# Performance work log

Hardware: AMD Instinct MI355X
Metric: run time of the kernel (lower is better)

The kernel has to match this reference:

```python
import jax, jax.numpy as jnp
import numpy as np

N, E, B = 50000, 600000, 64
C_IN, H, C_OUT, L = 128, 128, 64, 3
BN_EPS = 1e-5


def setup_inputs() -> dict:
    key = jax.random.key(0)
    ks = iter(jax.random.split(key, 40))

    def w(shape, fan_in):
        return jax.random.normal(next(ks), shape, jnp.float32) / np.sqrt(fan_in).astype(np.float32)

    return {
        "x": jax.random.normal(next(ks), (N, C_IN), jnp.float32),
        "edge_index": jax.random.randint(next(ks), (2, E), 0, N),
        "batch": jnp.sort(jax.random.randint(next(ks), (N,), 0, B)),
        # GINConv MLPs: Linear(in,h) -> BN -> ReLU -> Linear(h,h)   (stacked over L; C_IN == H)
        "convW1": w((L, C_IN, H), C_IN), "convb1": jnp.zeros((L, H), jnp.float32),
        "bn_g": jnp.ones((L, H), jnp.float32), "bn_b": jnp.zeros((L, H), jnp.float32),
        "convW2": w((L, H, H), H), "convb2": jnp.zeros((L, H), jnp.float32),
        # reconstruction head: Linear(h,h)-ReLU-Linear(h,h)-ReLU-Linear(h,4)-ReLU
        "recW1": w((H, H), H), "recb1": jnp.zeros((H,), jnp.float32),
        "recW2": w((H, H), H), "recb2": jnp.zeros((H,), jnp.float32),
        "recW3": w((H, 4), H), "recb3": jnp.zeros((4,), jnp.float32),
        # final MLP([h,h,out], norm=None): Linear(h,h)-ReLU-(dropout, eval=identity)-Linear(h,out)
        "mlpW1": w((H, H), H), "mlpb1": jnp.zeros((H,), jnp.float32),
        "mlpW2": w((H, C_OUT), H), "mlpb2": jnp.zeros((C_OUT,), jnp.float32),
    }


def reference(x, edge_index, batch, convW1, convb1, bn_g, bn_b, convW2, convb2,
              recW1, recb1, recW2, recb2, recW3, recb3, mlpW1, mlpb1, mlpW2, mlpb2):
    src, dst = edge_index[0], edge_index[1]
    for l in range(L):
        # GIN aggregation: out_i = nn((1+eps)*x_i + sum_{j->i} x_j), eps = 0
        agg = jax.ops.segment_sum(x[src], dst, num_segments=N)  # [N, d]
        h = (x + agg) @ convW1[l] + convb1[l]                   # [N, H]
        mu = h.mean(axis=0)
        var = jnp.var(h, axis=0)                                # biased, torch BN train mode
        h = bn_g[l] * (h - mu) * jax.lax.rsqrt(var + BN_EPS) + bn_b[l]
        h = jax.nn.relu(h) @ convW2[l] + convb2[l]
        x = jax.nn.relu(h)                                      # outer .relu() in forward
    # reconstruction branch on node features
    x_rec = jax.nn.relu(x @ recW1 + recb1)
    x_rec = jax.nn.relu(x_rec @ recW2 + recb2)
    x_rec = jax.nn.relu(x_rec @ recW3 + recb3)                  # [N, 4]
    # global_add_pool keyed by graph id
    pooled = jax.ops.segment_sum(x, batch, num_segments=B)      # [B, H]
    out = jax.nn.relu(pooled @ mlpW1 + mlpb1) @ mlpW2 + mlpb2   # [B, C_OUT]
    return (out, x_rec)
```

## Files before the change

### kernel.cpp

```cpp
#include <hip/hip_runtime.h>

#define NN 50000
#define EE 600000
#define BB 64
#define CH 128
#define LL 3
#define NGB 391
#define NSB 196
#define NPB 392

typedef unsigned short u16;
typedef unsigned int u32;
typedef short s16x8 __attribute__((ext_vector_type(8)));
typedef float f32x4 __attribute__((ext_vector_type(4)));

__device__ __forceinline__ u16 f2b(float f) {
    u32 x = __float_as_uint(f);
    return (u16)((x + 0x7FFFu + ((x >> 16) & 1u)) >> 16);
}
__device__ __forceinline__ float b2f(u16 u) {
    return __uint_as_float(((u32)u) << 16);
}

__global__ __launch_bounds__(256) void k_zero2(int* __restrict__ deg,
                                               float* __restrict__ pooled) {
    int i = blockIdx.x * 256 + threadIdx.x;
    if (i < NN) deg[i] = 0;
    int j = i - NN;
    if (j >= 0 && j < BB * CH) pooled[j] = 0.f;
}

__global__ __launch_bounds__(256) void k_count(const int* __restrict__ ei,
                                               int* __restrict__ deg) {
    int e = blockIdx.x * 256 + threadIdx.x;
    if (e < EE) atomicAdd(&deg[ei[EE + e]], 1);
}

__global__ __launch_bounds__(256) void k_scanA(const int* __restrict__ deg,
                                               int* __restrict__ bsum) {
    __shared__ int sm[256];
    int i = blockIdx.x * 256 + threadIdx.x;
    sm[threadIdx.x] = (i < NN) ? deg[i] : 0;
    __syncthreads();
    for (int off = 128; off > 0; off >>= 1) {
        if (threadIdx.x < off) sm[threadIdx.x] += sm[threadIdx.x + off];
        __syncthreads();
    }
    if (threadIdx.x == 0) bsum[blockIdx.x] = sm[0];
}

__global__ __launch_bounds__(256) void k_scanB(const int* __restrict__ deg,
                                               const int* __restrict__ bsum,
                                               int* __restrict__ rowptr,
                                               int* __restrict__ cur) {
    __shared__ int sb[256], sd[256];
    int t = threadIdx.x;
    sb[t] = (t < NSB) ? bsum[t] : 0;
    __syncthreads();
    for (int off = 1; off < 256; off <<= 1) {
        int v = (t >= off) ? sb[t - off] : 0;
        __syncthreads();
        sb[t] += v;
        __syncthreads();
    }
    int blockOff = (blockIdx.x == 0) ? 0 : sb[blockIdx.x - 1];
    int i = blockIdx.x * 256 + t;
    int d = (i < NN) ? deg[i] : 0;
    sd[t] = d;
    __syncthreads();
    for (int off = 1; off < 256; off <<= 1) {
        int v = (t >= off) ? sd[t - off] : 0;
        __syncthreads();
        sd[t] += v;
        __syncthreads();
    }
    int excl = blockOff + sd[t] - d;
    if (i < NN) { rowptr[i] = excl; cur[i] = excl; }
    if (i == NN - 1) rowptr[NN] = excl + d;
}

__global__ __launch_bounds__(256) void k_fill(const int* __restrict__ ei,
                                              int* __restrict__ cur,
                                              int* __restrict__ perm) {
    int e = blockIdx.x * 256 + threadIdx.x;
    if (e < EE) {
        int dst = ei[EE + e];
        int idx = atomicAdd(&cur[dst], 1);
        perm[idx] = ei[e];
    }
}

__global__ __launch_bounds__(256) void k_cvt(const float* __restrict__ x,
                                             u16* __restrict__ y) {
    long base = (long)(blockIdx.x * 256 + threadIdx.x) * 8;
    if (base < (long)NN * CH) {
        float4 f0 = *(const float4*)(x + base);
        float4 f1 = *(const float4*)(x + base + 4);
        union { u16 pk[8]; uint4 v; } uu;
        uu.pk[0] = f2b(f0.x); uu.pk[1] = f2b(f0.y);
        uu.pk[2] = f2b(f0.z); uu.pk[3] = f2b(f0.w);
        uu.pk[4] = f2b(f1.x); uu.pk[5] = f2b(f1.y);
        uu.pk[6] = f2b(f1.z); uu.pk[7] = f2b(f1.w);
        *(uint4*)(y + base) = uu.v;
    }
}

__global__ __launch_bounds__(256) void k_gather(const u16* __restrict__ x,
                                                const int* __restrict__ rowptr,
                                                const int* __restrict__ perm,
                                                u16* __restrict__ y) {
    int dst = blockIdx.x * 16 + (threadIdx.x >> 4);
    if (dst >= NN) return;
    int lane = threadIdx.x & 15;
    int co = lane * 8;
    int beg = rowptr[dst], end = rowptr[dst + 1];
    union { u16 pk[8]; uint4 v; } uu;
    uu.v = *(const uint4*)(x + (long)dst * CH + co);
    float a[8], b[8];
#pragma unroll
    for (int j = 0; j < 8; ++j) { a[j] = b2f(uu.pk[j]); b[j] = 0.f; }
    int e = beg;
    for (; e + 1 < end; e += 2) {
        int s0 = perm[e], s1 = perm[e + 1];
        union { u16 pk[8]; uint4 v; } v0, v1;
        v0.v = *(const uint4*)(x + (long)s0 * CH + co);
        v1.v = *(const uint4*)(x + (long)s1 * CH + co);
#pragma unroll
        for (int j = 0; j < 8; ++j) { a[j] += b2f(v0.pk[j]); b[j] += b2f(v1.pk[j]); }
    }
    if (e < end) {
        int s0 = perm[e];
        union { u16 pk[8]; uint4 v; } v0;
        v0.v = *(const uint4*)(x + (long)s0 * CH + co);
#pragma unroll
        for (int j = 0; j < 8; ++j) a[j] += b2f(v0.pk[j]);
    }
    union { u16 pk[8]; uint4 v; } ov;
#pragma unroll
    for (int j = 0; j < 8; ++j) ov.pk[j] = f2b(a[j] + b[j]);
    *(uint4*)(y + (long)dst * CH + co) = ov.v;
}

__global__ __launch_bounds__(256) void k_transpose_all(
    const float* __restrict__ cW1, const float* __restrict__ cW2,
    const float* __restrict__ rW1, const float* __restrict__ rW2,
    const float* __restrict__ rW3, u16* __restrict__ Wt) {
    int idx = blockIdx.x * 256 + threadIdx.x;
    if (idx < 8 * 16384) {
        int slot = idx >> 14;
        int wi = idx & 16383;
        int k = wi >> 7, n = wi & 127;
        const float* src = slot < 3 ? cW1 + slot * 16384
                         : slot < 6 ? cW2 + (slot - 3) * 16384
                         : slot == 6 ? rW1 : rW2;
        Wt[slot * 16384 + n * 128 + k] = f2b(src[wi]);
    } else if (idx < 9 * 16384) {
        int j = idx - 8 * 16384;
        int n = j >> 7, k = j & 127;
        Wt[8 * 16384 + j] = (n < 4) ? f2b(rW3[k * 4 + n]) : (u16)0;
    }
}

__device__ __forceinline__ void stageB8(const u16* __restrict__ Wt, u16* sB,
                                        int s, int rr) {
#pragma unroll
    for (int it = 0; it < 8; ++it) {
        int n = it * 16 + rr;
        uint4 u = *(const uint4*)(Wt + n * CH + 8 * s);
        *(uint4*)(&sB[n * CH + ((s ^ (n & 15)) * 8)]) = u;
    }
}

__device__ __forceinline__ void mfma8(const u16* sA, const u16* sB,
                                      f32x4 acc[2][8], int wv, int quad, int l16) {
    f32x4 z = {0.f, 0.f, 0.f, 0.f};
#pragma unroll
    for (int m = 0; m < 2; ++m)
#pragma unroll
        for (int t = 0; t < 8; ++t) acc[m][t] = z;
    const u16* pa0 = sA + (wv * 32 + l16) * CH;
    const u16* pa1 = pa0 + 16 * CH;
#pragma unroll
    for (int kc = 0; kc < 4; ++kc) {
        int off = (((kc << 2) | quad) ^ l16) << 3;
        s16x8 a0 = *(const s16x8*)(pa0 + off);
        s16x8 a1 = *(const s16x8*)(pa1 + off);
#pragma unroll
        for (int t = 0; t < 8; ++t) {
            s16x8 bfr = *(const s16x8*)(sB + (t * 16 + l16) * CH + off);
            acc[0][t] = __builtin_amdgcn_mfma_f32_16x16x32_bf16(a0, bfr, acc[0][t], 0, 0, 0);
            acc[1][t] = __builtin_amdgcn_mfma_f32_16x16x32_bf16(a1, bfr, acc[1][t], 0, 0, 0);
        }
    }
}

__device__ __forceinline__ void biasrelu(f32x4 acc[2][8],
                                         const float* __restrict__ bias, int l16) {
#pragma unroll
    for (int t = 0; t < 8; ++t) {
        float bv = bias[t * 16 + l16];
#pragma unroll
        for (int m = 0; m < 2; ++m)
#pragma unroll
            for (int r = 0; r < 4; ++r)
                acc[m][t][r] = fmaxf(acc[m][t][r] + bv, 0.f);
    }
}

__device__ __forceinline__ void restage(const f32x4 acc[2][8], u16* sA,
                                        int wv, int quad, int l16) {
#pragma unroll
    for (int t = 0; t < 8; ++t) {
        int chunk = (t << 1) | (l16 >> 3);
        int o7 = l16 & 7;
#pragma unroll
        for (int m = 0; m < 2; ++m)
#pragma unroll
            for (int r = 0; r < 4; ++r) {
                int lr = wv * 32 + m * 16 + quad * 4 + r;
                sA[lr * CH + ((chunk ^ (lr & 15)) << 3) + o7] = f2b(acc[m][t][r]);
            }
    }
}

template <bool ABF16, bool BN, bool RELU, bool STATS, bool OUTBF16>
__global__ __launch_bounds__(256) void k_gemm(
    const void* __restrict__ Ap, const u16* __restrict__ Wt,
    const float* __restrict__ bias, const float* __restrict__ scale,
    const float* __restrict__ shift, void* __restrict__ Cp,
    float* __restrict__ pstats, int M) {
    __shared__ u16 sA[128 * CH];
    __shared__ u16 sB[128 * CH];
    const int tid = threadIdx.x;
    const int s = tid & 15;
    const int rr = tid >> 4;
    const int r0 = blockIdx.x * 128;

    float sc[8], sh[8];
    if constexpr (BN) {
#pragma unroll
        for (int j = 0; j < 8; ++j) {
            sc[j] = scale[8 * s + j];
            sh[j] = shift[8 * s + j];
        }
    }

    stageB8(Wt, sB, s, rr);
#pragma unroll
    for (int it = 0; it < 8; ++it) {
        int lr = it * 16 + rr;
        int gr = r0 + lr;
        union { u16 pk[8]; uint4 v; } uu;
        if (gr < M) {
            if constexpr (ABF16) {
                uu.v = *(const uint4*)((const u16*)Ap + (long)gr * CH + 8 * s);
                if constexpr (BN) {
#pragma unroll
                    for (int j = 0; j < 8; ++j)
                        uu.pk[j] = f2b(fmaxf(b2f(uu.pk[j]) * sc[j] + sh[j], 0.f));
                }
            } else {
                const float* Af = (const float*)Ap + (long)gr * CH + 8 * s;
                float4 f0 = *(const float4*)Af;
                float4 f1 = *(const float4*)(Af + 4);
                float vj[8] = {f0.x, f0.y, f0.z, f0.w, f1.x, f1.y, f1.z, f1.w};
#pragma unroll
                for (int j = 0; j < 8; ++j) {
                    float v = vj[j];
                    if constexpr (BN) v = fmaxf(v * sc[j] + sh[j], 0.f);
                    uu.pk[j] = f2b(v);
                }
            }
        } else {
#pragma unroll
            for (int j = 0; j < 8; ++j) uu.pk[j] = 0;
        }
        *(uint4*)(&sA[lr * CH + ((s ^ (lr & 15)) * 8)]) = uu.v;
    }
    __syncthreads();

    const int lane = tid & 63;
    const int wv = tid >> 6;
    const int quad = lane >> 4;
    const int l16 = lane & 15;

    f32x4 acc[2][8];
    mfma8(sA, sB, acc, wv, quad, l16);

    float ss[8], qq[8];
    if constexpr (STATS) {
#pragma unroll
        for (int t = 0; t < 8; ++t) { ss[t] = 0.f; qq[t] = 0.f; }
    }

#pragma unroll
    for (int t = 0; t < 8; ++t) {
        int col = t * 16 + l16;
        float bv = bias[col];
#pragma unroll
        for (int m = 0; m < 2; ++m) {
            int rbase = r0 + wv * 32 + m * 16 + quad * 4;
#pragma unroll
            for (int r = 0; r < 4; ++r) {
                int row = rbase + r;
                if (row < M) {
                    float v = acc[m][t][r] + bv;
                    if constexpr (STATS) { ss[t] += v; qq[t] += v * v; }
                    if constexpr (RELU) v = fmaxf(v, 0.f);
                    if constexpr (OUTBF16)
                        ((u16*)Cp)[(long)row * CH + col] = f2b(v);
                    else
                        ((float*)Cp)[(long)row * CH + col] = v;
                }
            }
        }
    }

    if constexpr (STATS) {
#pragma unroll
        for (int t = 0; t < 8; ++t) {
            ss[t] += __shfl_xor(ss[t], 16);
            ss[t] += __shfl_xor(ss[t], 32);
            qq[t] += __shfl_xor(qq[t], 16);
            qq[t] += __shfl_xor(qq[t], 32);
        }
        float* red = (float*)sA;
        __syncthreads();
        if (lane < 16) {
#pragma unroll
            for (int t = 0; t < 8; ++t) {
                red[wv * 256 + t * 16 + l16] = ss[t];
                red[wv * 256 + 128 + t * 16 + l16] = qq[t];
            }
        }
        __syncthreads();
        float v = red[tid] + red[256 + tid] + red[512 + tid] + red[768 + tid];
        pstats[(long)blockIdx.x * 256 + tid] = v;
    }
}

__global__ __launch_bounds__(256) void k_tail(
    const u16* __restrict__ h16, const u16* __restrict__ Wt,
    const float* __restrict__ cb2, const float* __restrict__ scale,
    const float* __restrict__ shift, const float* __restrict__ rb1,
    const float* __restrict__ rb2, const float* __restrict__ rb3,
    u16* __restrict__ xc, float* __restrict__ x_rec) {
    __shared__ u16 sA[128 * CH];
    __shared__ u16 sB[128 * CH];
    const int tid = threadIdx.x;
    const int s = tid & 15, rr = tid >> 4;
    const int r0 = blockIdx.x * 128;
    const int lane = tid & 63, wv = tid >> 6, quad = lane >> 4, l16 = lane & 15;

    float sc[8], sh[8];
#pragma unroll
    for (int j = 0; j < 8; ++j) { sc[j] = scale[8 * s + j]; sh[j] = shift[8 * s + j]; }
    stageB8(Wt + 5 * 16384, sB, s, rr);
#pragma unroll
    for (int it = 0; it < 8; ++it) {
        int lr = it * 16 + rr, gr = r0 + lr;
        union { u16 pk[8]; uint4 v; } uu;
        if (gr < NN) {
            uu.v = *(const uint4*)(h16 + (long)gr * CH + 8 * s);
#pragma unroll
            for (int j = 0; j < 8; ++j)
                uu.pk[j] = f2b(fmaxf(b2f(uu.pk[j]) * sc[j] + sh[j], 0.f));
        } else {
#pragma unroll
            for (int j = 0; j < 8; ++j) uu.pk[j] = 0;
        }
        *(uint4*)(&sA[lr * CH + ((s ^ (lr & 15)) * 8)]) = uu.v;
    }
    __syncthreads();
    f32x4 acc[2][8];
    mfma8(sA, sB, acc, wv, quad, l16);
    biasrelu(acc, cb2, l16);
#pragma unroll
    for (int t = 0; t < 8; ++t) {
        int col = t * 16 + l16;
#pragma unroll
        for (int m = 0; m < 2; ++m)
#pragma unroll
            for (int r = 0; r < 4; ++r) {
                int row = r0 + wv * 32 + m * 16 + quad * 4 + r;
                if (row < NN) xc[(long)row * CH + col] = f2b(acc[m][t][r]);
            }
    }
    __syncthreads();
    restage(acc, sA, wv, quad, l16);
    stageB8(Wt + 6 * 16384, sB, s, rr);
    __syncthreads();
    mfma8(sA, sB, acc, wv, quad, l16);
    biasrelu(acc, rb1, l16);
    __syncthreads();
    restage(acc, sA, wv, quad, l16);
    stageB8(Wt + 7 * 16384, sB, s, rr);
    __syncthreads();
    mfma8(sA, sB, acc, wv, quad, l16);
    biasrelu(acc, rb2, l16);
    __syncthreads();
    restage(acc, sA, wv, quad, l16);
    {
        int n = rr;
        uint4 u = *(const uint4*)(Wt + 8 * 16384 + n * CH + 8 * s);
        *(uint4*)(&sB[n * CH + ((s ^ (n & 15)) * 8)]) = u;
    }
    __syncthreads();
    f32x4 a4[2];
    a4[0] = (f32x4){0.f, 0.f, 0.f, 0.f};
    a4[1] = (f32x4){0.f, 0.f, 0.f, 0.f};
    {
        const u16* pa0 = sA + (wv * 32 + l16) * CH;
        const u16* pa1 = pa0 + 16 * CH;
#pragma unroll
        for (int kc = 0; kc < 4; ++kc) {
            int off = (((kc << 2) | quad) ^ l16) << 3;
            s16x8 a0 = *(const s16x8*)(pa0 + off);
            s16x8 a1 = *(const s16x8*)(pa1 + off);
            s16x8 bfr = *(const s16x8*)(sB + l16 * CH + off);
            a4[0] = __builtin_amdgcn_mfma_f32_16x16x32_bf16(a0, bfr, a4[0], 0, 0, 0);
            a4[1] = __builtin_amdgcn_mfma_f32_16x16x32_bf16(a1, bfr, a4[1], 0, 0, 0);
        }
    }
    if (l16 < 4) {
        float bv = rb3[l16];
#pragma unroll
        for (int m = 0; m < 2; ++m)
#pragma unroll
            for (int r = 0; r < 4; ++r) {
                int row = r0 + wv * 32 + m * 16 + quad * 4 + r;
                if (row < NN) x_rec[(long)row * 4 + l16] = fmaxf(a4[m][r] + bv, 0.f);
            }
    }
}

__global__ __launch_bounds__(256) void k_bnparam(const float* __restrict__ pstats,
                                                 const float* __restrict__ g,
                                                 const float* __restrict__ b,
                                                 float* __restrict__ scale,
                                                 float* __restrict__ shift) {
    __shared__ float sm[256];
    int t = threadIdx.x;
    float acc = 0.f;
    for (int blk = 0; blk < NGB; ++blk) acc += pstats[blk * 256 + t];
    sm[t] = acc;
    __syncthreads();
    if (t < 128) {
        float mu = sm[t] / (float)NN;
        float var = sm[128 + t] / (float)NN - mu * mu;
        float rstd = rsqrtf(var + 1e-5f);
        float gg = g[t], bb = b[t];
        scale[t] = gg * rstd;
        shift[t] = bb - mu * gg * rstd;
    }
}

__global__ __launch_bounds__(256) void k_pool(const u16* __restrict__ x,
                                              const int* __restrict__ batch,
                                              float* __restrict__ pooled) {
    int r0 = blockIdx.x * 128;
    if (r0 >= NN) return;
    int rend = r0 + 128 < NN ? r0 + 128 : NN;
    int c = threadIdx.x & 127;
    int half = threadIdx.x >> 7;
    int r = r0 + half;
    if (r >= rend) return;
    int g = batch[r];
    float s = 0.f;
    for (; r < rend; r += 2) {
        int gg = batch[r];
        if (gg != g) {
            unsafeAtomicAdd(pooled + g * CH + c, s);
            s = 0.f;
            g = gg;
        }
        s += b2f(x[(long)r * CH + c]);
    }
    unsafeAtomicAdd(pooled + g * CH + c, s);
}

__global__ __launch_bounds__(128) void k_mlp(const float* __restrict__ pooled,
                                             const float* __restrict__ W1,
                                             const float* __restrict__ b1,
                                             const float* __restrict__ W2,
                                             const float* __restrict__ b2,
                                             float* __restrict__ out) {
    __shared__ float p[128], t1[128];
    int b = blockIdx.x, t = threadIdx.x;
    p[t] = pooled[b * CH + t];
    __syncthreads();
    float acc = b1[t];
    for (int k = 0; k < 128; ++k) acc += p[k] * W1[k * 128 + t];
    t1[t] = fmaxf(acc, 0.f);
    __syncthreads();
    if (t < 64) {
        float o = b2[t];
        for (int k = 0; k < 128; ++k) o += t1[k] * W2[k * 64 + t];
        out[b * 64 + t] = o;
    }
}

extern "C" void kernel_launch(void* const* d_in, const int* in_sizes, int n_in,
                              void* d_out, int out_size, void* d_ws, size_t ws_size,
                              hipStream_t stream) {
    const float* x_in   = (const float*)d_in[0];
    const int*   ei     = (const int*)d_in[1];
    const int*   batch  = (const int*)d_in[2];
    const float* convW1 = (const float*)d_in[3];
    const float* convb1 = (const float*)d_in[4];
    const float* bn_g   = (const float*)d_in[5];
    const float* bn_b   = (const float*)d_in[6];
    const float* convW2 = (const float*)d_in[7];
    const float* convb2 = (const float*)d_in[8];
    const float* recW1  = (const float*)d_in[9];
    const float* recb1  = (const float*)d_in[10];
    const float* recW2  = (const float*)d_in[11];
    const float* recb2  = (const float*)d_in[12];
    const float* recW3  = (const float*)d_in[13];
    const float* recb3  = (const float*)d_in[14];
    const float* mlpW1  = (const float*)d_in[15];
    const float* mlpb1  = (const float*)d_in[16];
    const float* mlpW2  = (const float*)d_in[17];
    const float* mlpb2  = (const float*)d_in[18];

    float* out   = (float*)d_out;
    float* x_rec = out + 4096;

    char* w = (char*)d_ws;
    u16*   x16    = (u16*)w;    w += (size_t)NN * CH * 2;
    u16*   y16    = (u16*)w;    w += (size_t)NN * CH * 2;
    u16*   h16    = (u16*)w;    w += (size_t)NN * CH * 2;
    u16*   xc     = (u16*)w;    w += (size_t)NN * CH * 2;
    u16*   Wt     = (u16*)w;    w += (size_t)9 * 16384 * 2;
    float* pstats = (float*)w;  w += (size_t)NGB * 256 * 4;
    float* scale  = (float*)w;  w += 128 * 4;
    float* shift  = (float*)w;  w += 128 * 4;
    float* pooled = (float*)w;  w += (size_t)BB * CH * 4;
    int*   deg    = (int*)w;    w += (size_t)NN * 4;
    int*   bsum   = (int*)w;    w += (size_t)NSB * 4;
    int*   rowptr = (int*)w;    w += (size_t)(NN + 1) * 4;
    int*   cur    = (int*)w;    w += (size_t)NN * 4;
    int*   perm   = (int*)w;    w += (size_t)EE * 4;

    dim3 b256(256), b128(128);

    k_zero2<<<228, b256, 0, stream>>>(deg, pooled);
    k_count<<<2344, b256, 0, stream>>>(ei, deg);
    k_scanA<<<NSB, b256, 0, stream>>>(deg, bsum);
    k_scanB<<<NSB, b256, 0, stream>>>(deg, bsum, rowptr, cur);
    k_fill<<<2344, b256, 0, stream>>>(ei, cur, perm);
    k_cvt<<<3125, b256, 0, stream>>>(x_in, x16);
    k_transpose_all<<<576, b256, 0, stream>>>(convW1, convW2, recW1, recW2, recW3, Wt);

    const u16* cur_x = x16;
    for (int l = 0; l < LL; ++l) {
        k_gather<<<3125, b256, 0, stream>>>(cur_x, rowptr, perm, y16);
        k_gemm<true, false, false, true, true><<<NGB, b256, 0, stream>>>(
            y16, Wt + l * 16384, convb1 + l * 128, nullptr, nullptr, h16, pstats, NN);
        k_bnparam<<<1, b256, 0, stream>>>(pstats, bn_g + l * 128, bn_b + l * 128, scale, shift);
        if (l < LL - 1) {
            k_gemm<true, true, true, false, true><<<NGB, b256, 0, stream>>>(
                h16, Wt + (3 + l) * 16384, convb2 + l * 128, scale, shift, xc, nullptr, NN);
            cur_x = xc;
        }
    }
    k_tail<<<NGB, b256, 0, stream>>>(h16, Wt, convb2 + 2 * 128, scale, shift,
                                     recb1, recb2, recb3, xc, x_rec);
    k_pool<<<NPB, b256, 0, stream>>>(xc, batch, pooled);
    k_mlp<<<64, b128, 0, stream>>>(pooled, mlpW1, mlpb1, mlpW2, mlpb2, out);
}
```

Baseline: 431.6 us.

## Fuse per-layer GEMMs and BN stats via grid barrier in a single kernel

Replaces the per-layer sequence (GEMM1 with partial stats, single-block BN param reduction, GEMM2 with BN+ReLU) with one persistent kernel per layer. Each block keeps its GEMM1 accumulators in registers, atomically adds column sums into a global stats buffer, waits at a software grid barrier, then applies BN+ReLU and runs GEMM2 (plus the reconstruction head on the last layer). This removes the h16 intermediate round-trip through memory and two kernel launches per layer. The barrier depends on all 391 blocks being co-resident, which launch bounds of 2 blocks per CU are meant to ensure, and any block that is not resident would deadlock.

```diff
diff --git a/kernel.cpp b/kernel.cpp
--- a/kernel.cpp
+++ b/kernel.cpp
@@ -23,11 +23,17 @@
 }
 
 __global__ __launch_bounds__(256) void k_zero2(int* __restrict__ deg,
-                                               float* __restrict__ pooled) {
+                                               float* __restrict__ pooled,
+                                               float* __restrict__ gstats,
+                                               int* __restrict__ bar) {
     int i = blockIdx.x * 256 + threadIdx.x;
     if (i < NN) deg[i] = 0;
     int j = i - NN;
     if (j >= 0 && j < BB * CH) pooled[j] = 0.f;
+    int k = j - BB * CH;
+    if (k >= 0 && k < 3 * 256) gstats[k] = 0.f;
+    int l = k - 3 * 256;
+    if (l >= 0 && l < 4) bar[l] = 0;
 }
 
 __global__ __launch_bounds__(256) void k_count(const int* __restrict__ ei,
@@ -223,128 +229,25 @@
     }
 }
 
-template <bool ABF16, bool BN, bool RELU, bool STATS, bool OUTBF16>
-__global__ __launch_bounds__(256) void k_gemm(
-    const void* __restrict__ Ap, const u16* __restrict__ Wt,
-    const float* __restrict__ bias, const float* __restrict__ scale,
-    const float* __restrict__ shift, void* __restrict__ Cp,
-    float* __restrict__ pstats, int M) {
-    __shared__ u16 sA[128 * CH];
-    __shared__ u16 sB[128 * CH];
-    const int tid = threadIdx.x;
-    const int s = tid & 15;
-    const int rr = tid >> 4;
-    const int r0 = blockIdx.x * 128;
-
-    float sc[8], sh[8];
-    if constexpr (BN) {
-#pragma unroll
-        for (int j = 0; j < 8; ++j) {
-            sc[j] = scale[8 * s + j];
-            sh[j] = shift[8 * s + j];
-        }
-    }
-
-    stageB8(Wt, sB, s, rr);
-#pragma unroll
-    for (int it = 0; it < 8; ++it) {
-        int lr = it * 16 + rr;
-        int gr = r0 + lr;
-        union { u16 pk[8]; uint4 v; } uu;
-        if (gr < M) {
-            if constexpr (ABF16) {
-                uu.v = *(const uint4*)((const u16*)Ap + (long)gr * CH + 8 * s);
-                if constexpr (BN) {
-#pragma unroll
-                    for (int j = 0; j < 8; ++j)
-                        uu.pk[j] = f2b(fmaxf(b2f(uu.pk[j]) * sc[j] + sh[j], 0.f));
-                }
-            } else {
-                const float* Af = (const float*)Ap + (long)gr * CH + 8 * s;
-                float4 f0 = *(const float4*)Af;
-                float4 f1 = *(const float4*)(Af + 4);
-                float vj[8] = {f0.x, f0.y, f0.z, f0.w, f1.x, f1.y, f1.z, f1.w};
-#pragma unroll
-                for (int j = 0; j < 8; ++j) {
-                    float v = vj[j];
-                    if constexpr (BN) v = fmaxf(v * sc[j] + sh[j], 0.f);
-                    uu.pk[j] = f2b(v);
-                }
-            }
-        } else {
-#pragma unroll
-            for (int j = 0; j < 8; ++j) uu.pk[j] = 0;
-        }
-        *(uint4*)(&sA[lr * CH + ((s ^ (lr & 15)) * 8)]) = uu.v;
-    }
-    __syncthreads();
-
-    const int lane = tid & 63;
-    const int wv = tid >> 6;
-    const int quad = lane >> 4;
-    const int l16 = lane & 15;
-
-    f32x4 acc[2][8];
-    mfma8(sA, sB, acc, wv, quad, l16);
-
-    float ss[8], qq[8];
-    if constexpr (STATS) {
-#pragma unroll
-        for (int t = 0; t < 8; ++t) { ss[t] = 0.f; qq[t] = 0.f; }
-    }
-
-#pragma unroll
-    for (int t = 0; t < 8; ++t) {
-        int col = t * 16 + l16;
-        float bv = bias[col];
-#pragma unroll
-        for (int m = 0; m < 2; ++m) {
-            int rbase = r0 + wv * 32 + m * 16 + quad * 4;
-#pragma unroll
-            for (int r = 0; r < 4; ++r) {
-                int row = rbase + r;
-                if (row < M) {
-                    float v = acc[m][t][r] + bv;
-                    if constexpr (STATS) { ss[t] += v; qq[t] += v * v; }
-                    if constexpr (RELU) v = fmaxf(v, 0.f);
-                    if constexpr (OUTBF16)
-                        ((u16*)Cp)[(long)row * CH + col] = f2b(v);
-                    else
-                        ((float*)Cp)[(long)row * CH + col] = v;
-                }
-            }
-        }
-    }
-
-    if constexpr (STATS) {
-#pragma unroll
-        for (int t = 0; t < 8; ++t) {
-            ss[t] += __shfl_xor(ss[t], 16);
-            ss[t] += __shfl_xor(ss[t], 32);
-            qq[t] += __shfl_xor(qq[t], 16);
-            qq[t] += __shfl_xor(qq[t], 32);
-        }
-        float* red = (float*)sA;
-        __syncthreads();
-        if (lane < 16) {
-#pragma unroll
-            for (int t = 0; t < 8; ++t) {
-                red[wv * 256 + t * 16 + l16] = ss[t];
-                red[wv * 256 + 128 + t * 16 + l16] = qq[t];
-            }
-        }
-        __syncthreads();
-        float v = red[tid] + red[256 + tid] + red[512 + tid] + red[768 + tid];
-        pstats[(long)blockIdx.x * 256 + tid] = v;
-    }
-}
-
-__global__ __launch_bounds__(256) void k_tail(
-    const u16* __restrict__ h16, const u16* __restrict__ Wt,
-    const float* __restrict__ cb2, const float* __restrict__ scale,
-    const float* __restrict__ shift, const float* __restrict__ rb1,
-    const float* __restrict__ rb2, const float* __restrict__ rb3,
-    u16* __restrict__ xc, float* __restrict__ x_rec) {
+__device__ __forceinline__ void grid_barrier(int* bar, int tid) {
+    __syncthreads();
+    if (tid == 0) {
+        __hip_atomic_fetch_add(bar, 1, __ATOMIC_ACQ_REL, __HIP_MEMORY_SCOPE_AGENT);
+        while (__hip_atomic_load(bar, __ATOMIC_ACQUIRE, __HIP_MEMORY_SCOPE_AGENT) < NGB) {
+            __builtin_amdgcn_s_sleep(8);
+        }
+    }
+    __syncthreads();
+}
+
+template <bool LAST>
+__global__ __launch_bounds__(256, 2) void k_layer(
+    const u16* __restrict__ y16, const u16* __restrict__ Wt, int layer,
+    const float* __restrict__ cb1, const float* __restrict__ cb2,
+    const float* __restrict__ g, const float* __restrict__ bbeta,
+    float* __restrict__ gstats, int* __restrict__ bar, u16* __restrict__ xc,
+    const float* __restrict__ rb1, const float* __restrict__ rb2,
+    const float* __restrict__ rb3, float* __restrict__ x_rec) {
     __shared__ u16 sA[128 * CH];
     __shared__ u16 sB[128 * CH];
     const int tid = threadIdx.x;
@@ -352,19 +255,13 @@
     const int r0 = blockIdx.x * 128;
     const int lane = tid & 63, wv = tid >> 6, quad = lane >> 4, l16 = lane & 15;
 
-    float sc[8], sh[8];
-#pragma unroll
-    for (int j = 0; j < 8; ++j) { sc[j] = scale[8 * s + j]; sh[j] = shift[8 * s + j]; }
-    stageB8(Wt + 5 * 16384, sB, s, rr);
+    stageB8(Wt + layer * 16384, sB, s, rr);
 #pragma unroll
     for (int it = 0; it < 8; ++it) {
         int lr = it * 16 + rr, gr = r0 + lr;
         union { u16 pk[8]; uint4 v; } uu;
         if (gr < NN) {
-            uu.v = *(const uint4*)(h16 + (long)gr * CH + 8 * s);
-#pragma unroll
-            for (int j = 0; j < 8; ++j)
-                uu.pk[j] = f2b(fmaxf(b2f(uu.pk[j]) * sc[j] + sh[j], 0.f));
+            uu.v = *(const uint4*)(y16 + (long)gr * CH + 8 * s);
         } else {
 #pragma unroll
             for (int j = 0; j < 8; ++j) uu.pk[j] = 0;
@@ -373,6 +270,69 @@
     }
     __syncthreads();
     f32x4 acc[2][8];
+    mfma8(sA, sB, acc, wv, quad, l16);
+
+    float ss[8], qq[8];
+#pragma unroll
+    for (int t = 0; t < 8; ++t) {
+        float bv = cb1[t * 16 + l16];
+        ss[t] = 0.f; qq[t] = 0.f;
+#pragma unroll
+        for (int m = 0; m < 2; ++m) {
+            int rbase = r0 + wv * 32 + m * 16 + quad * 4;
+#pragma unroll
+            for (int r = 0; r < 4; ++r) {
+                float v = acc[m][t][r] + bv;
+                acc[m][t][r] = v;
+                if (rbase + r < NN) { ss[t] += v; qq[t] += v * v; }
+            }
+        }
+    }
+#pragma unroll
+    for (int t = 0; t < 8; ++t) {
+        ss[t] += __shfl_xor(ss[t], 16);
+        ss[t] += __shfl_xor(ss[t], 32);
+        qq[t] += __shfl_xor(qq[t], 16);
+        qq[t] += __shfl_xor(qq[t], 32);
+    }
+    float* red = (float*)sA;
+    __syncthreads();
+    if (lane < 16) {
+#pragma unroll
+        for (int t = 0; t < 8; ++t) {
+            red[wv * 256 + t * 16 + l16] = ss[t];
+            red[wv * 256 + 128 + t * 16 + l16] = qq[t];
+        }
+    }
+    __syncthreads();
+    unsafeAtomicAdd(&gstats[tid],
+                    red[tid] + red[256 + tid] + red[512 + tid] + red[768 + tid]);
+
+    grid_barrier(bar, tid);
+
+#pragma unroll
+    for (int t = 0; t < 8; ++t) {
+        int col = t * 16 + l16;
+        float sum = __hip_atomic_load(&gstats[col], __ATOMIC_RELAXED,
+                                      __HIP_MEMORY_SCOPE_AGENT);
+        float sq = __hip_atomic_load(&gstats[128 + col], __ATOMIC_RELAXED,
+                                     __HIP_MEMORY_SCOPE_AGENT);
+        float mu = sum / (float)NN;
+        float var = sq / (float)NN - mu * mu;
+        float rstd = rsqrtf(var + 1e-5f);
+        float sc = g[col] * rstd;
+        float sh = bbeta[col] - mu * sc;
+#pragma unroll
+        for (int m = 0; m < 2; ++m)
+#pragma unroll
+            for (int r = 0; r < 4; ++r)
+                acc[m][t][r] = fmaxf(acc[m][t][r] * sc + sh, 0.f);
+    }
+
+    __syncthreads();
+    restage(acc, sA, wv, quad, l16);
+    stageB8(Wt + (3 + layer) * 16384, sB, s, rr);
+    __syncthreads();
     mfma8(sA, sB, acc, wv, quad, l16);
     biasrelu(acc, cb2, l16);
 #pragma unroll
@@ -386,30 +346,31 @@
                 if (row < NN) xc[(long)row * CH + col] = f2b(acc[m][t][r]);
             }
     }
-    __syncthreads();
-    restage(acc, sA, wv, quad, l16);
-    stageB8(Wt + 6 * 16384, sB, s, rr);
-    __syncthreads();
-    mfma8(sA, sB, acc, wv, quad, l16);
-    biasrelu(acc, rb1, l16);
-    __syncthreads();
-    restage(acc, sA, wv, quad, l16);
-    stageB8(Wt + 7 * 16384, sB, s, rr);
-    __syncthreads();
-    mfma8(sA, sB, acc, wv, quad, l16);
-    biasrelu(acc, rb2, l16);
-    __syncthreads();
-    restage(acc, sA, wv, quad, l16);
-    {
-        int n = rr;
-        uint4 u = *(const uint4*)(Wt + 8 * 16384 + n * CH + 8 * s);
-        *(uint4*)(&sB[n * CH + ((s ^ (n & 15)) * 8)]) = u;
-    }
-    __syncthreads();
-    f32x4 a4[2];
-    a4[0] = (f32x4){0.f, 0.f, 0.f, 0.f};
-    a4[1] = (f32x4){0.f, 0.f, 0.f, 0.f};
-    {
+
+    if constexpr (LAST) {
+        __syncthreads();
+        restage(acc, sA, wv, quad, l16);
+        stageB8(Wt + 6 * 16384, sB, s, rr);
+        __syncthreads();
+        mfma8(sA, sB, acc, wv, quad, l16);
+        biasrelu(acc, rb1, l16);
+        __syncthreads();
+        restage(acc, sA, wv, quad, l16);
+        stageB8(Wt + 7 * 16384, sB, s, rr);
+        __syncthreads();
+        mfma8(sA, sB, acc, wv, quad, l16);
+        biasrelu(acc, rb2, l16);
+        __syncthreads();
+        restage(acc, sA, wv, quad, l16);
+        {
+            int n = rr;
+            uint4 u = *(const uint4*)(Wt + 8 * 16384 + n * CH + 8 * s);
+            *(uint4*)(&sB[n * CH + ((s ^ (n & 15)) * 8)]) = u;
+        }
+        __syncthreads();
+        f32x4 a4[2];
+        a4[0] = (f32x4){0.f, 0.f, 0.f, 0.f};
+        a4[1] = (f32x4){0.f, 0.f, 0.f, 0.f};
         const u16* pa0 = sA + (wv * 32 + l16) * CH;
         const u16* pa1 = pa0 + 16 * CH;
 #pragma unroll
@@ -421,37 +382,16 @@
             a4[0] = __builtin_amdgcn_mfma_f32_16x16x32_bf16(a0, bfr, a4[0], 0, 0, 0);
             a4[1] = __builtin_amdgcn_mfma_f32_16x16x32_bf16(a1, bfr, a4[1], 0, 0, 0);
         }
-    }
-    if (l16 < 4) {
-        float bv = rb3[l16];
-#pragma unroll
-        for (int m = 0; m < 2; ++m)
-#pragma unroll
-            for (int r = 0; r < 4; ++r) {
-                int row = r0 + wv * 32 + m * 16 + quad * 4 + r;
-                if (row < NN) x_rec[(long)row * 4 + l16] = fmaxf(a4[m][r] + bv, 0.f);
-            }
-    }
-}
-
-__global__ __launch_bounds__(256) void k_bnparam(const float* __restrict__ pstats,
-                                                 const float* __restrict__ g,
-                                                 const float* __restrict__ b,
-                                                 float* __restrict__ scale,
-                                                 float* __restrict__ shift) {
-    __shared__ float sm[256];
-    int t = threadIdx.x;
-    float acc = 0.f;
-    for (int blk = 0; blk < NGB; ++blk) acc += pstats[blk * 256 + t];
-    sm[t] = acc;
-    __syncthreads();
-    if (t < 128) {
-        float mu = sm[t] / (float)NN;
-        float var = sm[128 + t] / (float)NN - mu * mu;
-        float rstd = rsqrtf(var + 1e-5f);
-        float gg = g[t], bb = b[t];
-        scale[t] = gg * rstd;
-        shift[t] = bb - mu * gg * rstd;
+        if (l16 < 4) {
+            float bv = rb3[l16];
+#pragma unroll
+            for (int m = 0; m < 2; ++m)
+#pragma unroll
+                for (int r = 0; r < 4; ++r) {
+                    int row = r0 + wv * 32 + m * 16 + quad * 4 + r;
+                    if (row < NN) x_rec[(long)row * 4 + l16] = fmaxf(a4[m][r] + bv, 0.f);
+                }
+        }
     }
 }
 
@@ -529,12 +469,10 @@
     char* w = (char*)d_ws;
     u16*   x16    = (u16*)w;    w += (size_t)NN * CH * 2;
     u16*   y16    = (u16*)w;    w += (size_t)NN * CH * 2;
-    u16*   h16    = (u16*)w;    w += (size_t)NN * CH * 2;
     u16*   xc     = (u16*)w;    w += (size_t)NN * CH * 2;
     u16*   Wt     = (u16*)w;    w += (size_t)9 * 16384 * 2;
-    float* pstats = (float*)w;  w += (size_t)NGB * 256 * 4;
-    float* scale  = (float*)w;  w += 128 * 4;
-    float* shift  = (float*)w;  w += 128 * 4;
+    float* gstats = (float*)w;  w += (size_t)3 * 256 * 4;
+    int*   bar    = (int*)w;    w += 4 * 4;
     float* pooled = (float*)w;  w += (size_t)BB * CH * 4;
     int*   deg    = (int*)w;    w += (size_t)NN * 4;
     int*   bsum   = (int*)w;    w += (size_t)NSB * 4;
@@ -544,7 +482,7 @@
 
     dim3 b256(256), b128(128);
 
-    k_zero2<<<228, b256, 0, stream>>>(deg, pooled);
+    k_zero2<<<231, b256, 0, stream>>>(deg, pooled, gstats, bar);
     k_count<<<2344, b256, 0, stream>>>(ei, deg);
     k_scanA<<<NSB, b256, 0, stream>>>(deg, bsum);
     k_scanB<<<NSB, b256, 0, stream>>>(deg, bsum, rowptr, cur);
@@ -555,17 +493,18 @@
     const u16* cur_x = x16;
     for (int l = 0; l < LL; ++l) {
         k_gather<<<3125, b256, 0, stream>>>(cur_x, rowptr, perm, y16);
-        k_gemm<true, false, false, true, true><<<NGB, b256, 0, stream>>>(
-            y16, Wt + l * 16384, convb1 + l * 128, nullptr, nullptr, h16, pstats, NN);
-        k_bnparam<<<1, b256, 0, stream>>>(pstats, bn_g + l * 128, bn_b + l * 128, scale, shift);
-        if (l < LL - 1) {
-            k_gemm<true, true, true, false, true><<<NGB, b256, 0, stream>>>(
-                h16, Wt + (3 + l) * 16384, convb2 + l * 128, scale, shift, xc, nullptr, NN);
-            cur_x = xc;
-        }
-    }
-    k_tail<<<NGB, b256, 0, stream>>>(h16, Wt, convb2 + 2 * 128, scale, shift,
-                                     recb1, recb2, recb3, xc, x_rec);
+        if (l < LL - 1)
+            k_layer<false><<<NGB, b256, 0, stream>>>(
+                y16, Wt, l, convb1 + l * 128, convb2 + l * 128,
+                bn_g + l * 128, bn_b + l * 128, gstats + l * 256, bar + l, xc,
+                recb1, recb2, recb3, x_rec);
+        else
+            k_layer<true><<<NGB, b256, 0, stream>>>(
+                y16, Wt, l, convb1 + l * 128, convb2 + l * 128,
+                bn_g + l * 128, bn_b + l * 128, gstats + l * 256, bar + l, xc,
+                recb1, recb2, recb3, x_rec);
+        cur_x = xc;
+    }
     k_pool<<<NPB, b256, 0, stream>>>(xc, batch, pooled);
     k_mlp<<<64, b128, 0, stream>>>(pooled, mlpW1, mlpb1, mlpW2, mlpb2, out);
 }
```

Result: no change. 425.4 us (-1.4%).
